# Kernel optimization log

Measured on AMD Instinct MI355X. Metric: run time of the kernel, lower is better.

The kernel has to match this reference:

```python
import jax, jax.numpy as jnp
import numpy as np

DIM = 2048
NUM_HEADS = 16
HEAD_DIM = DIM // NUM_HEADS
ROPE_BASE = 10000.0


def _rope_cache(seq_len):
    inv_freq = 1.0 / (ROPE_BASE ** (jnp.arange(0, HEAD_DIM, 2, dtype=jnp.float32) / HEAD_DIM))
    t = jnp.arange(seq_len, dtype=jnp.float32)
    freqs = jnp.einsum('i,j->ij', t, inv_freq)          # [S, HEAD_DIM//2]
    emb = jnp.concatenate([freqs, freqs], axis=-1)       # [S, HEAD_DIM]
    return jnp.cos(emb), jnp.sin(emb)


def _rotate_half(x):
    x1, x2 = jnp.split(x, 2, axis=-1)
    return jnp.concatenate([-x2, x1], axis=-1)


def setup_inputs() -> dict:
    key = jax.random.key(0)
    kx, kq, ko = jax.random.split(key, 3)
    B, S = 2, 2048
    x = jax.random.normal(kx, (B, S, DIM), dtype=jnp.float32)
    # torch nn.Linear(dim, 3*dim) weight has shape [3*dim, dim]; y = x @ W.T
    w_qkv = jax.random.normal(kq, (3 * DIM, DIM), dtype=jnp.float32) * (DIM ** -0.5)
    w_out = jax.random.normal(ko, (DIM, DIM), dtype=jnp.float32) * (DIM ** -0.5)
    return {"x": x, "w_qkv": w_qkv, "w_out": w_out}


def reference(x, w_qkv, w_out):
    B, S, _ = x.shape
    qkv = x @ w_qkv.T                                   # [B, S, 3*DIM]
    q, k, v = jnp.split(qkv, 3, axis=-1)
    def to_heads(t):
        return t.reshape(B, S, NUM_HEADS, HEAD_DIM).transpose(0, 2, 1, 3)  # [B, H, S, d]
    q, k, v = to_heads(q), to_heads(k), to_heads(v)

    cos, sin = _rope_cache(S)                           # [S, d]
    cos = cos[None, None, :, :]
    sin = sin[None, None, :, :]
    q = q * cos + _rotate_half(q) * sin
    k = k * cos + _rotate_half(k) * sin

    scale = HEAD_DIM ** -0.5
    scores = jnp.einsum('bhqd,bhkd->bhqk', q, k) * scale  # [B, H, S, S]
    causal = jnp.tril(jnp.ones((S, S), dtype=bool))
    scores = jnp.where(causal[None, None], scores, -jnp.inf)
    attn = jax.nn.softmax(scores, axis=-1)
    out = jnp.einsum('bhqk,bhkd->bhqd', attn, v)          # [B, H, S, d]
    out = out.transpose(0, 2, 1, 3).reshape(B, S, DIM)
    return out @ w_out.T
```

## Files before the change

### kernel.cpp

```cpp
#include <hip/hip_runtime.h>
#include <cstdint>
#include <cstddef>

#define NHEADS 16
#define HDIM   128
#define BATCH  2
#define SEQ    2048
#define DMODEL 2048
#define MTOT   (BATCH*SEQ)
#define NQKV   (3*DMODEL)

typedef __attribute__((ext_vector_type(8))) __bf16 bf16x8;
typedef __attribute__((ext_vector_type(4))) float f32x4;
typedef __attribute__((ext_vector_type(8))) unsigned short ushort8v;

__device__ __forceinline__ unsigned short f2bf(float f){
  __bf16 h = (__bf16)f;
  return __builtin_bit_cast(unsigned short, h);
}
__device__ __forceinline__ float bf2f(unsigned short s){
  return __uint_as_float(((uint32_t)s) << 16);
}
__device__ __forceinline__ void gload_lds16(const void* src, void* lds_base){
  __builtin_amdgcn_global_load_lds((const __attribute__((address_space(1))) unsigned int*)src,
                                   (__attribute__((address_space(3))) unsigned int*)lds_base,
                                   16, 0, 0);
}

template<int CTRL>
__device__ __forceinline__ float dppmv(float x){
  return __uint_as_float((unsigned)__builtin_amdgcn_update_dpp(
      0, (int)__float_as_uint(x), CTRL, 0xF, 0xF, true));
}
__device__ __forceinline__ float rmax16(float x){
  x = fmaxf(x, dppmv<0x128>(x));
  x = fmaxf(x, dppmv<0x124>(x));
  x = fmaxf(x, dppmv<0x122>(x));
  x = fmaxf(x, dppmv<0x121>(x));
  return x;
}
__device__ __forceinline__ float rsum16(float x){
  x += dppmv<0x128>(x);
  x += dppmv<0x124>(x);
  x += dppmv<0x122>(x);
  x += dppmv<0x121>(x);
  return x;
}

__global__ void cast3_kernel(const float* __restrict__ s0, unsigned short* __restrict__ d0, int n0,
                             const float* __restrict__ s1, unsigned short* __restrict__ d1, int n1,
                             const float* __restrict__ s2, unsigned short* __restrict__ d2, int n2,
                             float2* __restrict__ tab){
  {
    const int i = blockIdx.x*blockDim.x + threadIdx.x;
    if (i < SEQ*64){
      const int j = i & 63, s = i >> 6;
      const float inv = exp2f(-(float)j * (13.287712379549449f/64.f));
      float sn, cs;
      sincosf((float)s * inv, &sn, &cs);
      tab[i] = make_float2(cs, sn);
    }
  }
  const int stride = gridDim.x*blockDim.x*8;
  const int base = (blockIdx.x*blockDim.x + threadIdx.x)*8;
  #pragma unroll 1
  for (int a = 0; a < 3; ++a){
    const float* s = a==0 ? s0 : (a==1 ? s1 : s2);
    unsigned short* d = a==0 ? d0 : (a==1 ? d1 : d2);
    const int n = a==0 ? n0 : (a==1 ? n1 : n2);
    for (int i = base; i < n; i += stride){
      float4 x = *reinterpret_cast<const float4*>(s + i);
      float4 y = *reinterpret_cast<const float4*>(s + i + 4);
      ushort8v o;
      o[0]=f2bf(x.x); o[1]=f2bf(x.y); o[2]=f2bf(x.z); o[3]=f2bf(x.w);
      o[4]=f2bf(y.x); o[5]=f2bf(y.y); o[6]=f2bf(y.z); o[7]=f2bf(y.w);
      *reinterpret_cast<ushort8v*>(d + i) = o;
    }
  }
}

template<int MODE>
__global__ __launch_bounds__(512, 2) void gemm2(
    const unsigned short* __restrict__ A,
    const unsigned short* __restrict__ Bw,
    float* __restrict__ Cf,
    unsigned short* __restrict__ qo,
    unsigned short* __restrict__ ko,
    unsigned short* __restrict__ vo,
    const float2* __restrict__ rtab,
    int M, int N, int K)
{
  __shared__ __align__(16) unsigned short smem[49152];
  auto lds = reinterpret_cast<unsigned short (*)[3][128*64]>(smem);

  const int lane = threadIdx.x & 63;
  const int wid  = threadIdx.x >> 6;
  const int wm = wid >> 2, wn = wid & 3;
  const int hi = lane >> 4;
  const int l15 = lane & 15;

  const int nwg = gridDim.x * gridDim.y;
  const int bid = blockIdx.y * gridDim.x + blockIdx.x;
  const int swz = (bid & 7) * (nwg >> 3) + (bid >> 3);
  const int by = swz & 31;
  const int bx = swz >> 5;
  const int m0 = by * 128;
  const int n0 = bx * 256;

  const int NT = K >> 6;

  auto stage = [&](const unsigned short* base, int row0, int k0, int buf, int slot){
    const int rlo = wid << 4;
    #pragma unroll
    for (int i=0;i<2;++i){
      const int r = rlo + i*8 + (lane>>3);
      const int csrc = ((lane&7) ^ (lane>>3)) << 3;
      gload_lds16(base + (size_t)(row0 + r)*K + k0 + csrc,
                  &lds[buf][slot][(rlo + i*8)*64]);
    }
  };
  auto frag = [&](const unsigned short* h, int r, int s){
    return *reinterpret_cast<const bf16x8*>(h + r*64 + ((s ^ (r&7)) << 3));
  };

  f32x4 acc[4][4];
  #pragma unroll
  for (int i=0;i<4;++i)
    #pragma unroll
    for (int j=0;j<4;++j) acc[i][j] = (f32x4){0.f,0.f,0.f,0.f};

  stage(A,  m0,      0, 0, 0);
  stage(Bw, n0,      0, 0, 1);
  stage(Bw, n0+128,  0, 0, 2);
  if (NT > 1){
    stage(A, m0, 64, 1, 0);
    asm volatile("s_waitcnt vmcnt(2)" ::: "memory");
  } else {
    asm volatile("s_waitcnt vmcnt(0)" ::: "memory");
  }
  __builtin_amdgcn_sched_barrier(0);
  __builtin_amdgcn_s_barrier();

  bf16x8 Ar[4][2];
  bf16x8 Br[2][2];

  auto tile_body = [&](int kt, int cur){
    const int nxt = cur ^ 1;
    const unsigned short* Ah = &lds[cur][0][0];
    const unsigned short* Bh = &lds[cur][1 + (wn>>1)][0];
    const int rbase = (wn & 1) * 64;

    #pragma unroll
    for (int fm=0;fm<4;++fm)
      #pragma unroll
      for (int kk=0;kk<2;++kk)
        Ar[fm][kk] = frag(Ah, wm*64 + fm*16 + l15, kk*4 + hi);
    #pragma unroll
    for (int nf=0;nf<2;++nf)
      #pragma unroll
      for (int kk=0;kk<2;++kk)
        Br[nf][kk] = frag(Bh, rbase + nf*16 + l15, kk*4 + hi);
    if (kt+1 < NT){
      stage(Bw, n0,     (kt+1)*64, nxt, 1);
      stage(Bw, n0+128, (kt+1)*64, nxt, 2);
    }
    asm volatile("s_waitcnt lgkmcnt(8)" ::: "memory");
    __builtin_amdgcn_sched_barrier(0);
    __builtin_amdgcn_s_barrier();
    asm volatile("s_waitcnt lgkmcnt(0)" ::: "memory");
    __builtin_amdgcn_sched_barrier(0);
    __builtin_amdgcn_s_setprio(1);
    #pragma unroll
    for (int fm=0;fm<4;++fm){
      acc[fm][0] = __builtin_amdgcn_mfma_f32_16x16x32_bf16(Ar[fm][0], Br[0][0], acc[fm][0], 0,0,0);
      acc[fm][0] = __builtin_amdgcn_mfma_f32_16x16x32_bf16(Ar[fm][1], Br[0][1], acc[fm][0], 0,0,0);
      acc[fm][1] = __builtin_amdgcn_mfma_f32_16x16x32_bf16(Ar[fm][0], Br[1][0], acc[fm][1], 0,0,0);
      acc[fm][1] = __builtin_amdgcn_mfma_f32_16x16x32_bf16(Ar[fm][1], Br[1][1], acc[fm][1], 0,0,0);
    }
    __builtin_amdgcn_s_setprio(0);
    __builtin_amdgcn_sched_barrier(0);
    __builtin_amdgcn_s_barrier();

    #pragma unroll
    for (int nf=0;nf<2;++nf)
      #pragma unroll
      for (int kk=0;kk<2;++kk)
        Br[nf][kk] = frag(Bh, rbase + 32 + nf*16 + l15, kk*4 + hi);
    if (kt+2 < NT) stage(A, m0, (kt+2)*64, cur, 0);
    __builtin_amdgcn_sched_barrier(0);
    __builtin_amdgcn_s_barrier();
    asm volatile("s_waitcnt lgkmcnt(0)" ::: "memory");
    __builtin_amdgcn_sched_barrier(0);
    __builtin_amdgcn_s_setprio(1);
    #pragma unroll
    for (int fm=0;fm<4;++fm){
      acc[fm][2] = __builtin_amdgcn_mfma_f32_16x16x32_bf16(Ar[fm][0], Br[0][0], acc[fm][2], 0,0,0);
      acc[fm][2] = __builtin_amdgcn_mfma_f32_16x16x32_bf16(Ar[fm][1], Br[0][1], acc[fm][2], 0,0,0);
      acc[fm][3] = __builtin_amdgcn_mfma_f32_16x16x32_bf16(Ar[fm][0], Br[1][0], acc[fm][3], 0,0,0);
      acc[fm][3] = __builtin_amdgcn_mfma_f32_16x16x32_bf16(Ar[fm][1], Br[1][1], acc[fm][3], 0,0,0);
    }
    __builtin_amdgcn_s_setprio(0);
    if (kt+2 < NT)      asm volatile("s_waitcnt vmcnt(2)" ::: "memory");
    else if (kt+1 < NT) asm volatile("s_waitcnt vmcnt(0)" ::: "memory");
    __builtin_amdgcn_sched_barrier(0);
    __builtin_amdgcn_s_barrier();
  };

  for (int kt2 = 0; kt2 < NT; kt2 += 2){
    tile_body(kt2,     0);
    tile_body(kt2 + 1, 1);
  }

  if (MODE == 0 && (n0 >> 11) == 2){
    unsigned short* trsp = smem;
    #pragma unroll
    for (int fm=0;fm<4;++fm){
      const int srow = wm*64 + fm*16 + hi*4;
      #pragma unroll
      for (int p=0;p<4;++p){
        const int dcol = wn*64 + p*16 + l15;
        f32x4 v = acc[fm][p];
        ushort4 pk;
        pk.x=f2bf(v[0]); pk.y=f2bf(v[1]); pk.z=f2bf(v[2]); pk.w=f2bf(v[3]);
        *reinterpret_cast<ushort4*>(trsp + dcol*136 + srow) = pk;
      }
    }
    __syncthreads();
    const int bb  = m0 >> 11;
    const int ss0 = m0 & 2047;
    const size_t vrow = (size_t)(bb*2048 + (n0 - 4096));
    const int t = threadIdx.x;
    #pragma unroll
    for (int it=0; it<8; ++it){
      const int dl = it*32 + (t>>4);
      const int ch = t & 15;
      ushort8v val = *reinterpret_cast<const ushort8v*>(trsp + dl*136 + ch*8);
      *reinterpret_cast<ushort8v*>(vo + (vrow + dl)*SEQ + ss0 + ch*8) = val;
    }
  } else if (MODE == 0){
    unsigned short* trsp = smem;
    #pragma unroll
    for (int fm=0;fm<4;++fm){
      const int rowl = wm*64 + fm*16 + hi*4;
      #pragma unroll
      for (int p=0;p<4;++p){
        const int c = wn*64 + p*16 + l15;
        f32x4 v = acc[fm][p];
        #pragma unroll
        for (int r=0;r<4;++r) trsp[(rowl+r)*264 + c] = f2bf(v[r]);
      }
    }
    __syncthreads();
    const bool isq = (n0 >> 11) == 0;
    unsigned short* dst = isq ? qo : ko;
    const float QS = 0.08838834764831845f * 1.4426950408889634f;
    const int t = threadIdx.x;
    #pragma unroll
    for (int it=0; it<4; ++it){
      const int v = it*512 + t;
      const int rv = v >> 4;
      const int head = (v >> 3) & 1;
      const int jb = (v & 7) * 8;
      ushort8v a = *reinterpret_cast<const ushort8v*>(trsp + rv*264 + head*128 + jb);
      ushort8v b = *reinterpret_cast<const ushort8v*>(trsp + rv*264 + head*128 + 64 + jb);
      const int grow = m0 + rv;
      const int ss = grow & 2047, bb = grow >> 11;
      const int hh = ((n0 >> 7) & 15) + head;
      const float4* tb = reinterpret_cast<const float4*>(rtab + (size_t)ss*64 + jb);
      float csv[8], snv[8];
      #pragma unroll
      for (int q=0;q<4;++q){
        float4 tq = tb[q];
        csv[2*q]   = tq.x; snv[2*q]   = tq.y;
        csv[2*q+1] = tq.z; snv[2*q+1] = tq.w;
      }
      ushort8v o1, o2;
      #pragma unroll
      for (int e=0;e<8;++e){
        float x1 = bf2f(a[e]), x2 = bf2f(b[e]);
        float r1 = x1*csv[e] - x2*snv[e];
        float r2 = x2*csv[e] + x1*snv[e];
        if (isq){ r1 *= QS; r2 *= QS; }
        o1[e] = f2bf(r1); o2[e] = f2bf(r2);
      }
      unsigned short* base = dst + ((size_t)(bb*NHEADS+hh)*SEQ + ss)*HDIM;
      *reinterpret_cast<ushort8v*>(base + jb)      = o1;
      *reinterpret_cast<ushort8v*>(base + 64 + jb) = o2;
    }
  } else {
    #pragma unroll
    for (int fm=0;fm<4;++fm){
      const int row0 = m0 + wm*64 + fm*16 + (hi<<2);
      #pragma unroll
      for (int p=0;p<4;++p){
        const int col = n0 + wn*64 + p*16 + l15;
        f32x4 v = acc[fm][p];
        #pragma unroll
        for (int r=0;r<4;++r) Cf[(size_t)(row0+r)*N + col] = v[r];
      }
    }
  }
}

__global__ __launch_bounds__(256, 2) void gemm_op(
    const unsigned short* __restrict__ A,
    const unsigned short* __restrict__ Bw,
    float* __restrict__ Cf,
    int M, int N, int K)
{
  __shared__ __align__(16) unsigned short smem[2][2][128*64];
  const int lane = threadIdx.x & 63;
  const int wid  = threadIdx.x >> 6;
  const int wm = wid >> 1, wn = wid & 1;
  const int hi = lane >> 4;
  const int l15 = lane & 15;

  const int nwg = gridDim.x * gridDim.y;
  const int bid = blockIdx.y * gridDim.x + blockIdx.x;
  const int swz = (bid & 7) * (nwg >> 3) + (bid >> 3);
  const int by = swz & 31;
  const int bx = swz >> 5;
  const int m0 = by * 128;
  const int n0 = bx * 128;

  const int NT = K >> 6;

  auto stage = [&](const unsigned short* base, int row0, int k0, int buf, int slot){
    const int rlo = wid << 5;
    #pragma unroll
    for (int i=0;i<4;++i){
      const int r = rlo + i*8 + (lane>>3);
      const int csrc = ((lane&7) ^ (lane>>3)) << 3;
      gload_lds16(base + (size_t)(row0 + r)*K + k0 + csrc,
                  &smem[buf][slot][(rlo + i*8)*64]);
    }
  };
  auto frag = [&](const unsigned short* h, int r, int s){
    return *reinterpret_cast<const bf16x8*>(h + r*64 + ((s ^ (r&7)) << 3));
  };

  f32x4 acc[4][4];
  #pragma unroll
  for (int i=0;i<4;++i)
    #pragma unroll
    for (int j=0;j<4;++j) acc[i][j] = (f32x4){0.f,0.f,0.f,0.f};

  stage(A,  m0, 0, 0, 0);
  stage(Bw, n0, 0, 0, 1);
  if (NT > 1){
    stage(A, m0, 64, 1, 0);
    asm volatile("s_waitcnt vmcnt(4)" ::: "memory");
  } else {
    asm volatile("s_waitcnt vmcnt(0)" ::: "memory");
  }
  __builtin_amdgcn_sched_barrier(0);
  __builtin_amdgcn_s_barrier();

  bf16x8 Ar[4][2];
  bf16x8 Br[2][2];

  auto tile_body = [&](int kt, int cur){
    const int nxt = cur ^ 1;
    const unsigned short* Ah = &smem[cur][0][0];
    const unsigned short* Bh = &smem[cur][1][0];
    const int rbase = wn * 64;

    #pragma unroll
    for (int fm=0;fm<4;++fm)
      #pragma unroll
      for (int kk=0;kk<2;++kk)
        Ar[fm][kk] = frag(Ah, wm*64 + fm*16 + l15, kk*4 + hi);
    #pragma unroll
    for (int nf=0;nf<2;++nf)
      #pragma unroll
      for (int kk=0;kk<2;++kk)
        Br[nf][kk] = frag(Bh, rbase + nf*16 + l15, kk*4 + hi);
    if (kt+1 < NT) stage(Bw, n0, (kt+1)*64, nxt, 1);
    asm volatile("s_waitcnt lgkmcnt(8)" ::: "memory");
    __builtin_amdgcn_sched_barrier(0);
    __builtin_amdgcn_s_barrier();
    asm volatile("s_waitcnt lgkmcnt(0)" ::: "memory");
    __builtin_amdgcn_sched_barrier(0);
    __builtin_amdgcn_s_setprio(1);
    #pragma unroll
    for (int fm=0;fm<4;++fm){
      acc[fm][0] = __builtin_amdgcn_mfma_f32_16x16x32_bf16(Ar[fm][0], Br[0][0], acc[fm][0], 0,0,0);
      acc[fm][0] = __builtin_amdgcn_mfma_f32_16x16x32_bf16(Ar[fm][1], Br[0][1], acc[fm][0], 0,0,0);
      acc[fm][1] = __builtin_amdgcn_mfma_f32_16x16x32_bf16(Ar[fm][0], Br[1][0], acc[fm][1], 0,0,0);
      acc[fm][1] = __builtin_amdgcn_mfma_f32_16x16x32_bf16(Ar[fm][1], Br[1][1], acc[fm][1], 0,0,0);
    }
    __builtin_amdgcn_s_setprio(0);
    __builtin_amdgcn_sched_barrier(0);
    __builtin_amdgcn_s_barrier();

    #pragma unroll
    for (int nf=0;nf<2;++nf)
      #pragma unroll
      for (int kk=0;kk<2;++kk)
        Br[nf][kk] = frag(Bh, rbase + 32 + nf*16 + l15, kk*4 + hi);
    if (kt+2 < NT) stage(A, m0, (kt+2)*64, cur, 0);
    __builtin_amdgcn_sched_barrier(0);
    __builtin_amdgcn_s_barrier();
    asm volatile("s_waitcnt lgkmcnt(0)" ::: "memory");
    __builtin_amdgcn_sched_barrier(0);
    __builtin_amdgcn_s_setprio(1);
    #pragma unroll
    for (int fm=0;fm<4;++fm){
      acc[fm][2] = __builtin_amdgcn_mfma_f32_16x16x32_bf16(Ar[fm][0], Br[0][0], acc[fm][2], 0,0,0);
      acc[fm][2] = __builtin_amdgcn_mfma_f32_16x16x32_bf16(Ar[fm][1], Br[0][1], acc[fm][2], 0,0,0);
      acc[fm][3] = __builtin_amdgcn_mfma_f32_16x16x32_bf16(Ar[fm][0], Br[1][0], acc[fm][3], 0,0,0);
      acc[fm][3] = __builtin_amdgcn_mfma_f32_16x16x32_bf16(Ar[fm][1], Br[1][1], acc[fm][3], 0,0,0);
    }
    __builtin_amdgcn_s_setprio(0);
    if (kt+2 < NT)      asm volatile("s_waitcnt vmcnt(4)" ::: "memory");
    else if (kt+1 < NT) asm volatile("s_waitcnt vmcnt(0)" ::: "memory");
    __builtin_amdgcn_sched_barrier(0);
    __builtin_amdgcn_s_barrier();
  };

  for (int kt2 = 0; kt2 < NT; kt2 += 2){
    tile_body(kt2,     0);
    tile_body(kt2 + 1, 1);
  }

  #pragma unroll
  for (int fm=0;fm<4;++fm){
    const int row0 = m0 + wm*64 + fm*16 + (hi<<2);
    #pragma unroll
    for (int p=0;p<4;++p){
      const int col = n0 + wn*64 + p*16 + l15;
      f32x4 v = acc[fm][p];
      #pragma unroll
      for (int r=0;r<4;++r) Cf[(size_t)(row0+r)*N + col] = v[r];
    }
  }
}

__global__ __launch_bounds__(256, 2) void attn_kernel(
    const unsigned short* __restrict__ qh,
    const unsigned short* __restrict__ kh,
    const unsigned short* __restrict__ vT,
    unsigned short* __restrict__ ao)
{
  __shared__ __align__(16) unsigned short Ks[2][64*128];
  __shared__ __align__(16) unsigned short Vs[2][128*64];
  __shared__ __align__(16) unsigned short Ps[4][16*64];

  const int lane = threadIdx.x & 63;
  const int wid  = threadIdx.x >> 6;
  const int hi   = lane >> 4;
  const int l15  = lane & 15;
  const int pr = blockIdx.x;
  const int bh = blockIdx.y;
  const int b_ = bh >> 4, h_ = bh & 15;

  const unsigned short* Qb = qh + (size_t)bh * SEQ * HDIM;
  const unsigned short* Kb = kh + (size_t)bh * SEQ * HDIM;
  const unsigned short* Vb = vT + (size_t)bh * HDIM * SEQ;

  const int qrowf[2] = { pr*64 + wid*16, (31-pr)*64 + wid*16 };

  auto stageKV = [&](int kg, int buf){
    #pragma unroll
    for (int i=0;i<4;++i){
      const int r  = (wid*4+i)*4 + (lane>>4);
      const int cb = ((lane&15)<<4) ^ ((r&7)<<4);
      gload_lds16(Kb + (size_t)(kg*64 + r)*HDIM + (cb>>1), &Ks[buf][0] + (wid*4+i)*512);
    }
    #pragma unroll
    for (int i=0;i<4;++i){
      const int d  = (wid*4+i)*8 + (lane>>3);
      const int cb = ((lane&7)<<4) ^ ((d&7)<<4);
      gload_lds16(Vb + (size_t)d*SEQ + kg*64 + (cb>>1), &Vs[buf][0] + (wid*4+i)*512);
    }
  };

  bf16x8 qf[2][4];
  #pragma unroll
  for (int fi=0; fi<2; ++fi){
    const int qr = qrowf[fi] + l15;
    #pragma unroll
    for (int ks = 0; ks < 4; ++ks)
      qf[fi][ks] = *reinterpret_cast<const bf16x8*>(Qb + (size_t)qr*HDIM + ks*32 + hi*8);
  }

  f32x4 oacc[2][8];
  #pragma unroll
  for (int fi=0;fi<2;++fi)
    #pragma unroll
    for (int t=0;t<8;++t) oacc[fi][t] = (f32x4){0.f,0.f,0.f,0.f};
  float mrun[2][4], lrun[2][4];
  #pragma unroll
  for (int fi=0;fi<2;++fi)
    #pragma unroll
    for (int r=0;r<4;++r){ mrun[fi][r] = -3.0e38f; lrun[fi][r] = 0.f; }

  const int nkt = 32 - pr;

  stageKV(0, 0);
  __syncthreads();

  for (int kt = 0; kt < nkt; ++kt){
    const int cur = kt & 1;
    if (kt + 1 < nkt) stageKV(kt + 1, cur ^ 1);

    const bool lo_act = (kt <= pr);

    f32x4 sacc[2][4];
    #pragma unroll
    for (int fi=0;fi<2;++fi)
      #pragma unroll
      for (int nt=0;nt<4;++nt) sacc[fi][nt] = (f32x4){0.f,0.f,0.f,0.f};
    __builtin_amdgcn_s_setprio(1);
    #pragma unroll
    for (int nt=0;nt<4;++nt){
      const int krow = nt*16 + l15;
      bf16x8 kf[4];
      #pragma unroll
      for (int ks=0;ks<4;++ks){
        const int cb = (ks*64 + (hi<<4)) ^ ((krow&7)<<4);
        kf[ks] = *reinterpret_cast<const bf16x8*>(&Ks[cur][0] + krow*128 + (cb>>1));
      }
      #pragma unroll
      for (int ks=0;ks<4;++ks)
        sacc[1][nt] = __builtin_amdgcn_mfma_f32_16x16x32_bf16(qf[1][ks], kf[ks], sacc[1][nt], 0,0,0);
      if (lo_act){
        #pragma unroll
        for (int ks=0;ks<4;++ks)
          sacc[0][nt] = __builtin_amdgcn_mfma_f32_16x16x32_bf16(qf[0][ks], kf[ks], sacc[0][nt], 0,0,0);
      }
    }
    __builtin_amdgcn_s_setprio(0);

    char* pb = (char*)&Ps[wid][0];
    #pragma unroll
    for (int fi=0; fi<2; ++fi){
      if (fi == 0 && !lo_act) continue;

      if (kt*64 + 63 > qrowf[fi]){
        #pragma unroll
        for (int nt=0;nt<4;++nt){
          const int key = kt*64 + nt*16 + l15;
          #pragma unroll
          for (int r=0;r<4;++r){
            const int qr = qrowf[fi] + hi*4 + r;
            if (key > qr) sacc[fi][nt][r] = -1.0e30f;
          }
        }
      }

      float mx[4]; float need = 0.f;
      #pragma unroll
      for (int r=0;r<4;++r){
        float m_ = fmaxf(fmaxf(sacc[fi][0][r], sacc[fi][1][r]),
                         fmaxf(sacc[fi][2][r], sacc[fi][3][r]));
        m_ = rmax16(m_);
        mx[r] = m_;
        need = fmaxf(need, m_ - mrun[fi][r]);
      }
      if (!__all(need <= 8.0f)){
        float fac[4];
        #pragma unroll
        for (int r=0;r<4;++r){
          const float mnew = fmaxf(mrun[fi][r], mx[r]);
          fac[r] = exp2f(mrun[fi][r] - mnew);
          mrun[fi][r] = mnew;
          lrun[fi][r] *= fac[r];
        }
        #pragma unroll
        for (int t=0;t<8;++t)
          #pragma unroll
          for (int r=0;r<4;++r) oacc[fi][t][r] *= fac[r];
      }
      #pragma unroll
      for (int r=0;r<4;++r){
        float ps = 0.f;
        #pragma unroll
        for (int nt=0;nt<4;++nt){
          const float p = exp2f(sacc[fi][nt][r] - mrun[fi][r]);
          sacc[fi][nt][r] = p;
          ps += p;
        }
        ps = rsum16(ps);
        lrun[fi][r] += ps;
      }

      #pragma unroll
      for (int nt=0;nt<4;++nt){
        const int keyb = (nt*16 + l15) << 1;
        #pragma unroll
        for (int r=0;r<4;++r){
          const int prow = hi*4 + r;
          *(unsigned short*)(pb + prow*128 + (keyb ^ ((prow&7)<<4))) = f2bf(sacc[fi][nt][r]);
        }
      }
      asm volatile("s_waitcnt lgkmcnt(0)" ::: "memory");
      __builtin_amdgcn_sched_barrier(0);

      bf16x8 pa[2];
      {
        const int prow = l15;
        #pragma unroll
        for (int ks=0;ks<2;++ks){
          const int pcb = (ks*64 + (hi<<4)) ^ ((prow&7)<<4);
          pa[ks] = *reinterpret_cast<const bf16x8*>(pb + prow*128 + pcb);
        }
      }
      __builtin_amdgcn_s_setprio(1);
      #pragma unroll
      for (int ks=0;ks<2;++ks){
        #pragma unroll
        for (int t=0;t<8;++t){
          const int drow = t*16 + l15;
          const int vcb = (ks*64 + (hi<<4)) ^ ((drow&7)<<4);
          bf16x8 vb = *reinterpret_cast<const bf16x8*>(&Vs[cur][0] + drow*64 + (vcb>>1));
          oacc[fi][t] = __builtin_amdgcn_mfma_f32_16x16x32_bf16(pa[ks], vb, oacc[fi][t], 0,0,0);
        }
      }
      __builtin_amdgcn_s_setprio(0);
    }

    __syncthreads();
  }

  #pragma unroll
  for (int fi=0;fi<2;++fi){
    float linv[4];
    #pragma unroll
    for (int r=0;r<4;++r) linv[r] = 1.0f / lrun[fi][r];
    #pragma unroll
    for (int t=0;t<8;++t){
      const int col = h_*HDIM + t*16 + l15;
      #pragma unroll
      for (int r=0;r<4;++r){
        const int s_ = qrowf[fi] + hi*4 + r;
        ao[(size_t)(b_*SEQ + s_)*DMODEL + col] = f2bf(oacc[fi][t][r] * linv[r]);
      }
    }
  }
}

extern "C" void kernel_launch(void* const* d_in, const int* in_sizes, int n_in,
                              void* d_out, int out_size, void* d_ws, size_t ws_size,
                              hipStream_t stream)
{
  const float* x     = (const float*)d_in[0];
  const float* w_qkv = (const float*)d_in[1];
  const float* w_out = (const float*)d_in[2];
  float* out = (float*)d_out;

  unsigned short* xb    = (unsigned short*)d_ws;
  unsigned short* wqkvb = xb    + (size_t)MTOT*DMODEL;
  unsigned short* woutb = wqkvb + (size_t)NQKV*DMODEL;
  unsigned short* qhb   = woutb + (size_t)DMODEL*DMODEL;
  unsigned short* khb   = qhb   + (size_t)MTOT*DMODEL;
  unsigned short* vtb   = khb   + (size_t)MTOT*DMODEL;
  unsigned short* aob   = vtb   + (size_t)MTOT*DMODEL;
  float2* rtab          = (float2*)(aob + (size_t)MTOT*DMODEL);

  hipLaunchKernelGGL(cast3_kernel, dim3(1024), dim3(256), 0, stream,
                     x, xb, MTOT*DMODEL, w_qkv, wqkvb, NQKV*DMODEL, w_out, woutb, DMODEL*DMODEL,
                     rtab);
  hipLaunchKernelGGL((gemm2<0>), dim3(NQKV/256, MTOT/128), dim3(512), 0, stream,
                     xb, wqkvb, (float*)nullptr, qhb, khb, vtb, rtab, MTOT, NQKV, DMODEL);
  hipLaunchKernelGGL(attn_kernel, dim3(16, BATCH*NHEADS), dim3(256), 0, stream, qhb, khb, vtb, aob);
  hipLaunchKernelGGL(gemm_op, dim3(DMODEL/128, MTOT/128), dim3(256), 0, stream,
                     aob, woutb, out, MTOT, DMODEL, DMODEL);
}
```

Measured before the change: 250.1 us.

## Shrink GEMM K-tile to 32 for higher occupancy; share V fragments across row groups

The GEMM drops its K-tile from 64 to 32 and shrinks shared memory to fit more workgroups per CU (launch bounds 2 to 4). It replaces the split two-phase pipelined loop with a simpler double-buffered loop that waits on all outstanding loads every iteration. In the attention kernel, the PV MMA loop now runs once after both P fragments are loaded, so each V fragment read from shared memory serves both query row groups. The cost is twice as many barriers and full vmcnt waits per K step in the GEMM, plus tighter register limits at 4 waves per SIMD, which may cause spills.

```diff
diff --git a/kernel.cpp b/kernel.cpp
--- a/kernel.cpp
+++ b/kernel.cpp
@@ -80,7 +80,7 @@
 }
 
 template<int MODE>
-__global__ __launch_bounds__(512, 2) void gemm2(
+__global__ __launch_bounds__(512, 4) void gemm2(
     const unsigned short* __restrict__ A,
     const unsigned short* __restrict__ Bw,
     float* __restrict__ Cf,
@@ -90,8 +90,8 @@
     const float2* __restrict__ rtab,
     int M, int N, int K)
 {
-  __shared__ __align__(16) unsigned short smem[49152];
-  auto lds = reinterpret_cast<unsigned short (*)[3][128*64]>(smem);
+  __shared__ __align__(16) unsigned short smem[34816];
+  auto lds = reinterpret_cast<unsigned short (*)[3][128*32]>(smem);
 
   const int lane = threadIdx.x & 63;
   const int wid  = threadIdx.x >> 6;
@@ -107,20 +107,16 @@
   const int m0 = by * 128;
   const int n0 = bx * 256;
 
-  const int NT = K >> 6;
+  const int NT = K >> 5;
 
   auto stage = [&](const unsigned short* base, int row0, int k0, int buf, int slot){
-    const int rlo = wid << 4;
-    #pragma unroll
-    for (int i=0;i<2;++i){
-      const int r = rlo + i*8 + (lane>>3);
-      const int csrc = ((lane&7) ^ (lane>>3)) << 3;
-      gload_lds16(base + (size_t)(row0 + r)*K + k0 + csrc,
-                  &lds[buf][slot][(rlo + i*8)*64]);
-    }
+    const int r = threadIdx.x >> 2;
+    const int csrc = (((threadIdx.x & 3) ^ ((r>>1)&3)) << 3);
+    gload_lds16(base + (size_t)(row0 + r)*K + k0 + csrc,
+                &lds[buf][slot][wid*512]);
   };
   auto frag = [&](const unsigned short* h, int r, int s){
-    return *reinterpret_cast<const bf16x8*>(h + r*64 + ((s ^ (r&7)) << 3));
+    return *reinterpret_cast<const bf16x8*>(h + r*32 + ((s ^ ((r>>1)&3)) << 3));
   };
 
   f32x4 acc[4][4];
@@ -129,86 +125,42 @@
     #pragma unroll
     for (int j=0;j<4;++j) acc[i][j] = (f32x4){0.f,0.f,0.f,0.f};
 
-  stage(A,  m0,      0, 0, 0);
-  stage(Bw, n0,      0, 0, 1);
-  stage(Bw, n0+128,  0, 0, 2);
-  if (NT > 1){
-    stage(A, m0, 64, 1, 0);
-    asm volatile("s_waitcnt vmcnt(2)" ::: "memory");
-  } else {
-    asm volatile("s_waitcnt vmcnt(0)" ::: "memory");
-  }
+  stage(A,  m0,     0, 0, 0);
+  stage(Bw, n0,     0, 0, 1);
+  stage(Bw, n0+128, 0, 0, 2);
+  asm volatile("s_waitcnt vmcnt(0)" ::: "memory");
   __builtin_amdgcn_sched_barrier(0);
   __builtin_amdgcn_s_barrier();
 
-  bf16x8 Ar[4][2];
-  bf16x8 Br[2][2];
-
-  auto tile_body = [&](int kt, int cur){
-    const int nxt = cur ^ 1;
+  bf16x8 Ar[4], Br[4];
+
+  for (int kt = 0; kt < NT; ++kt){
+    const int cur = kt & 1, nxt = cur ^ 1;
     const unsigned short* Ah = &lds[cur][0][0];
     const unsigned short* Bh = &lds[cur][1 + (wn>>1)][0];
     const int rbase = (wn & 1) * 64;
 
+    if (kt+1 < NT){
+      stage(A,  m0,     (kt+1)*32, nxt, 0);
+      stage(Bw, n0,     (kt+1)*32, nxt, 1);
+      stage(Bw, n0+128, (kt+1)*32, nxt, 2);
+    }
+    #pragma unroll
+    for (int fm=0;fm<4;++fm) Ar[fm] = frag(Ah, wm*64 + fm*16 + l15, hi);
+    #pragma unroll
+    for (int p=0;p<4;++p)    Br[p]  = frag(Bh, rbase + p*16 + l15, hi);
+    asm volatile("s_waitcnt lgkmcnt(0)" ::: "memory");
+    __builtin_amdgcn_sched_barrier(0);
+    __builtin_amdgcn_s_setprio(1);
     #pragma unroll
     for (int fm=0;fm<4;++fm)
       #pragma unroll
-      for (int kk=0;kk<2;++kk)
-        Ar[fm][kk] = frag(Ah, wm*64 + fm*16 + l15, kk*4 + hi);
-    #pragma unroll
-    for (int nf=0;nf<2;++nf)
-      #pragma unroll
-      for (int kk=0;kk<2;++kk)
-        Br[nf][kk] = frag(Bh, rbase + nf*16 + l15, kk*4 + hi);
-    if (kt+1 < NT){
-      stage(Bw, n0,     (kt+1)*64, nxt, 1);
-      stage(Bw, n0+128, (kt+1)*64, nxt, 2);
-    }
-    asm volatile("s_waitcnt lgkmcnt(8)" ::: "memory");
+      for (int p=0;p<4;++p)
+        acc[fm][p] = __builtin_amdgcn_mfma_f32_16x16x32_bf16(Ar[fm], Br[p], acc[fm][p], 0,0,0);
+    __builtin_amdgcn_s_setprio(0);
+    if (kt+1 < NT) asm volatile("s_waitcnt vmcnt(0)" ::: "memory");
     __builtin_amdgcn_sched_barrier(0);
     __builtin_amdgcn_s_barrier();
-    asm volatile("s_waitcnt lgkmcnt(0)" ::: "memory");
-    __builtin_amdgcn_sched_barrier(0);
-    __builtin_amdgcn_s_setprio(1);
-    #pragma unroll
-    for (int fm=0;fm<4;++fm){
-      acc[fm][0] = __builtin_amdgcn_mfma_f32_16x16x32_bf16(Ar[fm][0], Br[0][0], acc[fm][0], 0,0,0);
-      acc[fm][0] = __builtin_amdgcn_mfma_f32_16x16x32_bf16(Ar[fm][1], Br[0][1], acc[fm][0], 0,0,0);
-      acc[fm][1] = __builtin_amdgcn_mfma_f32_16x16x32_bf16(Ar[fm][0], Br[1][0], acc[fm][1], 0,0,0);
-      acc[fm][1] = __builtin_amdgcn_mfma_f32_16x16x32_bf16(Ar[fm][1], Br[1][1], acc[fm][1], 0,0,0);
-    }
-    __builtin_amdgcn_s_setprio(0);
-    __builtin_amdgcn_sched_barrier(0);
-    __builtin_amdgcn_s_barrier();
-
-    #pragma unroll
-    for (int nf=0;nf<2;++nf)
-      #pragma unroll
-      for (int kk=0;kk<2;++kk)
-        Br[nf][kk] = frag(Bh, rbase + 32 + nf*16 + l15, kk*4 + hi);
-    if (kt+2 < NT) stage(A, m0, (kt+2)*64, cur, 0);
-    __builtin_amdgcn_sched_barrier(0);
-    __builtin_amdgcn_s_barrier();
-    asm volatile("s_waitcnt lgkmcnt(0)" ::: "memory");
-    __builtin_amdgcn_sched_barrier(0);
-    __builtin_amdgcn_s_setprio(1);
-    #pragma unroll
-    for (int fm=0;fm<4;++fm){
-      acc[fm][2] = __builtin_amdgcn_mfma_f32_16x16x32_bf16(Ar[fm][0], Br[0][0], acc[fm][2], 0,0,0);
-      acc[fm][2] = __builtin_amdgcn_mfma_f32_16x16x32_bf16(Ar[fm][1], Br[0][1], acc[fm][2], 0,0,0);
-      acc[fm][3] = __builtin_amdgcn_mfma_f32_16x16x32_bf16(Ar[fm][0], Br[1][0], acc[fm][3], 0,0,0);
-      acc[fm][3] = __builtin_amdgcn_mfma_f32_16x16x32_bf16(Ar[fm][1], Br[1][1], acc[fm][3], 0,0,0);
-    }
-    __builtin_amdgcn_s_setprio(0);
-    if (kt+2 < NT)      asm volatile("s_waitcnt vmcnt(2)" ::: "memory");
-    else if (kt+1 < NT) asm volatile("s_waitcnt vmcnt(0)" ::: "memory");
-    __builtin_amdgcn_sched_barrier(0);
-    __builtin_amdgcn_s_barrier();
-  };
-
-  for (int kt2 = 0; kt2 < NT; kt2 += 2){
-    tile_body(kt2,     0);
-    tile_body(kt2 + 1, 1);
   }
 
   if (MODE == 0 && (n0 >> 11) == 2){
@@ -533,6 +485,7 @@
     __builtin_amdgcn_s_setprio(0);
 
     char* pb = (char*)&Ps[wid][0];
+    bf16x8 pa[2][2];
     #pragma unroll
     for (int fi=0; fi<2; ++fi){
       if (fi == 0 && !lo_act) continue;
@@ -597,28 +550,32 @@
       asm volatile("s_waitcnt lgkmcnt(0)" ::: "memory");
       __builtin_amdgcn_sched_barrier(0);
 
-      bf16x8 pa[2];
       {
         const int prow = l15;
         #pragma unroll
         for (int ks=0;ks<2;++ks){
           const int pcb = (ks*64 + (hi<<4)) ^ ((prow&7)<<4);
-          pa[ks] = *reinterpret_cast<const bf16x8*>(pb + prow*128 + pcb);
+          pa[fi][ks] = *reinterpret_cast<const bf16x8*>(pb + prow*128 + pcb);
         }
       }
-      __builtin_amdgcn_s_setprio(1);
-      #pragma unroll
-      for (int ks=0;ks<2;++ks){
-        #pragma unroll
-        for (int t=0;t<8;++t){
-          const int drow = t*16 + l15;
-          const int vcb = (ks*64 + (hi<<4)) ^ ((drow&7)<<4);
-          bf16x8 vb = *reinterpret_cast<const bf16x8*>(&Vs[cur][0] + drow*64 + (vcb>>1));
-          oacc[fi][t] = __builtin_amdgcn_mfma_f32_16x16x32_bf16(pa[ks], vb, oacc[fi][t], 0,0,0);
-        }
-      }
-      __builtin_amdgcn_s_setprio(0);
-    }
+      asm volatile("s_waitcnt lgkmcnt(0)" ::: "memory");
+      __builtin_amdgcn_sched_barrier(0);
+    }
+
+    __builtin_amdgcn_s_setprio(1);
+    #pragma unroll
+    for (int ks=0;ks<2;++ks){
+      #pragma unroll
+      for (int t=0;t<8;++t){
+        const int drow = t*16 + l15;
+        const int vcb = (ks*64 + (hi<<4)) ^ ((drow&7)<<4);
+        bf16x8 vb = *reinterpret_cast<const bf16x8*>(&Vs[cur][0] + drow*64 + (vcb>>1));
+        oacc[1][t] = __builtin_amdgcn_mfma_f32_16x16x32_bf16(pa[1][ks], vb, oacc[1][t], 0,0,0);
+        if (lo_act)
+          oacc[0][t] = __builtin_amdgcn_mfma_f32_16x16x32_bf16(pa[0][ks], vb, oacc[0][t], 0,0,0);
+      }
+    }
+    __builtin_amdgcn_s_setprio(0);
 
     __syncthreads();
   }
```

Result: slower. 264.1 us (+5.6%).
